# Kernel tuning notes

Measured on AMD Instinct MI355X. Metric: run time of the kernel, lower is better.

Reference implementation:

```python
import jax, jax.numpy as jnp
import numpy as np

N = 50000      # nodes
E = 600000     # edges
D_IN = 128
D = 128        # embedding_size
H = 2 * D      # GENConv MLP hidden (expansion=2, num_layers=2)
L = 6          # gnn_layers
OUT = 2        # out_channels
EPS_MSG = 1e-7   # GENConv message eps
EPS_SM = 1e-16   # PyG softmax denominator eps
LN_EPS = 1e-5


def setup_inputs() -> dict:
    key = jax.random.key(0)
    ks = jax.random.split(key, 18)
    s_in = 1.0 / np.sqrt(D_IN)
    s_d = 1.0 / np.sqrt(D)
    s_h = 1.0 / np.sqrt(H)
    return {
        "x": jax.random.normal(ks[0], (N, D_IN), jnp.float32),
        "edge_index": jax.random.randint(ks[1], (2, E), 0, N, jnp.int64),
        # node encoder
        "enc_W": jax.random.normal(ks[2], (D_IN, D), jnp.float32) * s_in,
        "enc_b": jnp.zeros((D,), jnp.float32),
        # per-layer DeepGCN params (stacked over L layers)
        "ln_g": jnp.ones((L, D), jnp.float32),
        "ln_b": jnp.zeros((L, D), jnp.float32),
        "t": jnp.ones((L,), jnp.float32),  # learnable softmax temperature
        "W1": jax.random.normal(ks[3], (L, D, H), jnp.float32) * s_d,
        "b1": jnp.zeros((L, H), jnp.float32),
        "mln_g": jnp.ones((L, H), jnp.float32),
        "mln_b": jnp.zeros((L, H), jnp.float32),
        "W2": jax.random.normal(ks[4], (L, H, D), jnp.float32) * s_h,
        "b2": jnp.zeros((L, D), jnp.float32),
        # final MLP head (linear_layers=2)
        "lin_W1": jax.random.normal(ks[5], (D, D), jnp.float32) * s_d,
        "lin_b1": jnp.zeros((D,), jnp.float32),
        "lin_W2": jax.random.normal(ks[6], (D, OUT), jnp.float32) * s_d,
        "lin_b2": jnp.zeros((OUT,), jnp.float32),
    }


def _layernorm(h, g, b):
    mu = jnp.mean(h, axis=-1, keepdims=True)
    var = jnp.mean(jnp.square(h - mu), axis=-1, keepdims=True)
    return (h - mu) * jax.lax.rsqrt(var + LN_EPS) * g + b


def _genconv(h, src, dst, t, W1, b1, mg, mb, W2, b2):
    """GENConv with softmax aggregation: gather -> segment softmax -> scatter -> MLP."""
    msg = jax.nn.relu(h[src]) + EPS_MSG            # [E, D]
    scaled = msg * t
    mmax = jax.ops.segment_max(scaled, dst, num_segments=N)  # [N, D]
    mmax = jnp.where(jnp.isfinite(mmax), mmax, 0.0)          # empty segments
    ex = jnp.exp(scaled - mmax[dst])                          # [E, D]
    denom = jax.ops.segment_sum(ex, dst, num_segments=N)     # [N, D]
    alpha = ex / (denom[dst] + EPS_SM)
    agg = jax.ops.segment_sum(msg * alpha, dst, num_segments=N)  # [N, D]
    out = agg + h                                  # root/self term
    z = out @ W1 + b1                              # [N, 2D]
    z = jax.nn.relu(_layernorm(z, mg, mb))
    return z @ W2 + b2                             # [N, D]


def reference(x, edge_index, enc_W, enc_b, ln_g, ln_b, t, W1, b1,
              mln_g, mln_b, W2, b2, lin_W1, lin_b1, lin_W2, lin_b2):
    src, dst = edge_index[0], edge_index[1]
    h = x @ enc_W + enc_b                          # node encoder [N, D]
    for i in range(L):                             # DeepGCNLayer 'res+' blocks
        g = _layernorm(h, ln_g[i], ln_b[i])
        g = jax.nn.relu(g)                         # (dropout: inference no-op)
        g = _genconv(g, src, dst, t[i], W1[i], b1[i], mln_g[i], mln_b[i], W2[i], b2[i])
        h = h + g
    h = jax.nn.relu(h @ lin_W1 + lin_b1)           # head (dropout_rate=None)
    return h @ lin_W2 + lin_b2                     # [N, OUT]
```

## Files before the change

### kernel.cpp

```cpp
#include <hip/hip_runtime.h>

#define NN 50000
#define EE 600000
#define DD 128
#define HH 256
#define LL 6
#define NB 49

typedef _Float16 f16x8 __attribute__((ext_vector_type(8)));
typedef float f32x4 __attribute__((ext_vector_type(4)));

__device__ __forceinline__ float bf2f(unsigned short u){
  unsigned int x = ((unsigned int)u) << 16; float f; __builtin_memcpy(&f, &x, 4); return f;
}
__device__ __forceinline__ unsigned short f2bf(float f){
  unsigned int x; __builtin_memcpy(&x, &f, 4);
  unsigned int lsb = (x >> 16) & 1u; x += 0x7fffu + lsb; return (unsigned short)(x >> 16);
}
__device__ __forceinline__ float wave_sum(float v){
  #pragma unroll
  for (int off = 32; off >= 1; off >>= 1) v += __shfl_xor(v, off, 64);
  return v;
}
__device__ __forceinline__ unsigned short f2h(float f){
  _Float16 h = (_Float16)f; unsigned short u; __builtin_memcpy(&u, &h, 2); return u;
}
__device__ __forceinline__ float h2f(unsigned short u){
  _Float16 h; __builtin_memcpy(&h, &u, 2); return (float)h;
}

__global__ void k_detect(const unsigned short* __restrict__ xh,
                         const unsigned int* __restrict__ ew,
                         int* __restrict__ flags){
  __shared__ int s_bad, s_nz;
  int t = threadIdx.x;
  if (t == 0){ s_bad = 0; s_nz = 0; }
  __syncthreads();
  int bad = 0;
  for (int i = t; i < 512; i += 256){
    unsigned e = (xh[i] >> 7) & 0xffu;
    if (e < 96u || e > 135u) bad = 1;
  }
  if (bad) atomicOr(&s_bad, 1);
  int nz = 0;
  for (int i = t; i < 1024; i += 256)
    if ((i & 1) && ew[i] != 0u) nz = 1;
  if (nz) atomicOr(&s_nz, 1);
  __syncthreads();
  if (t == 0){
    flags[0] = s_bad ? 1 : 0;
    flags[1] = s_nz ? 0 : 1;
  }
}

__global__ void k_cvt_edges(const void* __restrict__ ei, const int* __restrict__ flags,
                            int* __restrict__ s32, int* __restrict__ d32){
  int e = blockIdx.x*256 + threadIdx.x;
  if (e >= EE) return;
  int sv, dv;
  if (flags[1]){
    const long long* p = (const long long*)ei;
    sv = (int)p[e]; dv = (int)p[EE + e];
  } else {
    const int* p = (const int*)ei;
    sv = p[e]; dv = p[EE + e];
  }
  s32[e] = ((unsigned)sv < (unsigned)NN) ? sv : 0;
  d32[e] = ((unsigned)dv < (unsigned)NN) ? dv : 0;
}

__global__ void k_hist(const int* __restrict__ dst, int* __restrict__ deg){
  int e = blockIdx.x*256 + threadIdx.x;
  if (e < EE) atomicAdd(&deg[dst[e]], 1);
}

__global__ void k_blocksum(const int* __restrict__ deg, int* __restrict__ bsum){
  __shared__ int ws[4];
  int t = threadIdx.x, b = blockIdx.x;
  int s = 0;
  int i0 = b*1024 + t*4;
  #pragma unroll
  for (int j=0;j<4;j++){ int i = i0+j; if (i < NN) s += deg[i]; }
  #pragma unroll
  for (int off=32; off>=1; off>>=1) s += __shfl_xor(s, off, 64);
  if ((t&63)==0) ws[t>>6] = s;
  __syncthreads();
  if (t==0) bsum[b] = ws[0]+ws[1]+ws[2]+ws[3];
}

__global__ void k_scanb(const int* __restrict__ bsum, int* __restrict__ boff, int* __restrict__ rowptr){
  int lane = threadIdx.x;
  int v = (lane < NB) ? bsum[lane] : 0;
  int inc = v;
  #pragma unroll
  for (int off=1; off<64; off<<=1){ int u = __shfl_up(inc, off, 64); if (lane>=off) inc += u; }
  if (lane < NB) boff[lane] = inc - v;
  if (lane == 63) rowptr[NN] = inc;
}

__global__ void k_scanscatter(const int* __restrict__ deg, const int* __restrict__ boff,
                              int* __restrict__ rowptr, int* __restrict__ pos){
  __shared__ int ws[4];
  int t = threadIdx.x, b = blockIdx.x;
  int lane = t & 63, wid = t >> 6;
  int i0 = b*1024 + t*4;
  int d[4];
  #pragma unroll
  for (int j=0;j<4;j++){ int i=i0+j; d[j] = (i<NN)? deg[i] : 0; }
  int tot = d[0]+d[1]+d[2]+d[3];
  int inc = tot;
  #pragma unroll
  for (int off=1; off<64; off<<=1){ int u = __shfl_up(inc, off, 64); if (lane>=off) inc += u; }
  if (lane==63) ws[wid] = inc;
  __syncthreads();
  int woff = 0;
  for (int w=0; w<wid; w++) woff += ws[w];
  int base = boff[b] + woff + (inc - tot);
  int pre = 0;
  #pragma unroll
  for (int j=0;j<4;j++){
    int i = i0+j;
    if (i<NN){ rowptr[i] = base + pre; pos[i] = base + pre; }
    pre += d[j];
  }
}

__global__ void k_fill(const int* __restrict__ src, const int* __restrict__ dst,
                       int* __restrict__ pos, int* __restrict__ csr){
  int e = blockIdx.x*256 + threadIdx.x;
  if (e < EE){
    int d = dst[e];
    int p = atomicAdd(&pos[d], 1);
    csr[p] = src[e];
  }
}

__global__ void k_prep_w(const int* __restrict__ flags,
    const void* __restrict__ encW, const void* __restrict__ linW1,
    const void* __restrict__ W1, const void* __restrict__ W2,
    unsigned short* __restrict__ ph, unsigned short* __restrict__ pl)
{
  int idx = blockIdx.x*256 + threadIdx.x;
  int fp32 = flags[0];
  const void* src; int off;
  if (idx < 16384){ int n=idx>>7, k=idx&127; src=encW; off=k*128+n; }
  else if (idx < 32768){ int o=idx-16384; int n=o>>7, k=o&127; src=linW1; off=k*128+n; }
  else if (idx < 229376){ int o=idx-32768; int l=o>>15, r=o&32767; int n=r>>7, k=r&127; src=W1; off=l*32768+k*256+n; }
  else { int o=idx-229376; int l=o>>15, r=o&32767; int n=r>>8, k=r&255; src=W2; off=l*32768+k*128+n; }
  float w = fp32 ? ((const float*)src)[off] : bf2f(((const unsigned short*)src)[off]);
  unsigned short h = f2h(w);
  ph[idx] = h;
  pl[idx] = f2h(w - h2f(h));
}

#define SM_ENCB 0
#define SM_LNG 128
#define SM_LNB 896
#define SM_TV 1664
#define SM_B1 1670
#define SM_MG 3206
#define SM_MB 4742
#define SM_B2 6278
#define SM_LINB1 7046
#define SM_LINW2 7174
#define SM_LINB2 7430
#define SM_TOT 7432
__global__ void k_prep_small(const int* __restrict__ flags,
    const void* s0, const void* s1, const void* s2, const void* s3,
    const void* s4, const void* s5, const void* s6, const void* s7,
    const void* s8, const void* s9, const void* s10, float* __restrict__ out)
{
  int i = blockIdx.x*256 + threadIdx.x;
  if (i >= SM_TOT) return;
  int fp32 = flags[0];
  const void* src; int off;
  if      (i < SM_LNG)  { src=s0;  off=i; }
  else if (i < SM_LNB)  { src=s1;  off=i-SM_LNG; }
  else if (i < SM_TV)   { src=s2;  off=i-SM_LNB; }
  else if (i < SM_B1)   { src=s3;  off=i-SM_TV; }
  else if (i < SM_MG)   { src=s4;  off=i-SM_B1; }
  else if (i < SM_MB)   { src=s5;  off=i-SM_MG; }
  else if (i < SM_B2)   { src=s6;  off=i-SM_MB; }
  else if (i < SM_LINB1){ src=s7;  off=i-SM_B2; }
  else if (i < SM_LINW2){ src=s8;  off=i-SM_LINB1; }
  else if (i < SM_LINB2){ src=s9;  off=i-SM_LINW2; }
  else                  { src=s10; off=i-SM_LINB2; }
  out[i] = fp32 ? ((const float*)src)[off] : bf2f(((const unsigned short*)src)[off]);
}

__device__ __forceinline__ void emit_me(unsigned short* me, int row, int col, float g, float tv){
  float m = g + 1e-7f;
  me[(size_t)row*256 + col] = f2h(m);
  me[(size_t)row*256 + 128 + col] = f2h(__expf(fminf(m*tv, 18.f) - 8.f));
}

template<int EPI>
__global__ __launch_bounds__(256, 4) void k_gemm(const void* __restrict__ Ap,
    const unsigned short* __restrict__ WTh, const unsigned short* __restrict__ WTl,
    const float* __restrict__ bias, void* __restrict__ Cv,
    int M, const int* __restrict__ flags, int aExt)
{
  __shared__ __align__(16) char smem[27648];
  short* lA = (short*)smem;
  short* lW = (short*)(smem + 9216);
  short* hT = (short*)smem;

  const int tid = threadIdx.x, lane = tid & 63, wid = tid >> 6;
  const int mi = lane & 15, q = lane >> 4;
  const int rowb = blockIdx.x * 64;
  const int fp32m = flags[0];

  f32x4 acc[4][2];
  #pragma unroll
  for (int a=0;a<4;a++)
    #pragma unroll
    for (int c=0;c<2;c++){ acc[a][c][0]=0.f; acc[a][c][1]=0.f; acc[a][c][2]=0.f; acc[a][c][3]=0.f; }

  const int nW = fp32m ? 2 : 1;
  for (int pass = 0; pass < nW; ++pass){
    const unsigned short* Wp = pass ? WTl : WTh;
    for (int kc = 0; kc < 2; ++kc){
      {
        const int kv = (tid & 7) * 8, r0 = tid >> 3;
        #pragma unroll
        for (int p = 0; p < 2; ++p){
          int row = p*32 + r0, grow = rowb + row;
          uint4 d = make_uint4(0u,0u,0u,0u);
          if (grow < M){
            if (!aExt){
              d = *(const uint4*)((const unsigned short*)Ap + (size_t)grow*128 + kc*64 + kv);
            } else if (!fp32m){
              uint4 u = *(const uint4*)((const unsigned short*)Ap + (size_t)grow*128 + kc*64 + kv);
              const unsigned short* us = (const unsigned short*)&u;
              unsigned short hh[8];
              #pragma unroll
              for (int c=0;c<8;c++) hh[c] = f2h(bf2f(us[c]));
              d.x = hh[0]|((unsigned)hh[1]<<16); d.y = hh[2]|((unsigned)hh[3]<<16);
              d.z = hh[4]|((unsigned)hh[5]<<16); d.w = hh[6]|((unsigned)hh[7]<<16);
            } else {
              const float* fp = (const float*)Ap + (size_t)grow*128 + kc*64 + kv;
              float4 v0 = *(const float4*)fp, v1 = *(const float4*)(fp+4);
              unsigned short hh[8] = {f2h(v0.x),f2h(v0.y),f2h(v0.z),f2h(v0.w),
                                      f2h(v1.x),f2h(v1.y),f2h(v1.z),f2h(v1.w)};
              d.x = hh[0]|((unsigned)hh[1]<<16); d.y = hh[2]|((unsigned)hh[3]<<16);
              d.z = hh[4]|((unsigned)hh[5]<<16); d.w = hh[6]|((unsigned)hh[7]<<16);
            }
          }
          *(uint4*)&lA[row*72 + kv] = d;
        }
        #pragma unroll
        for (int p = 0; p < 4; ++p){
          int n = p*32 + (tid >> 3);
          *(uint4*)&lW[n*72 + (tid & 7)*8] = *(const uint4*)(Wp + (size_t)n*128 + kc*64 + (tid & 7)*8);
        }
      }
      __syncthreads();
      #pragma unroll
      for (int ks = 0; ks < 2; ++ks){
        const int koff = ks*32 + q*8;
        f16x8 af[4], bw[2];
        #pragma unroll
        for (int rt=0; rt<4; rt++) af[rt] = *(const f16x8*)&lA[(rt*16+mi)*72 + koff];
        #pragma unroll
        for (int ct=0; ct<2; ct++) bw[ct] = *(const f16x8*)&lW[(wid*32 + ct*16 + mi)*72 + koff];
        #pragma unroll
        for (int rt=0; rt<4; rt++)
          #pragma unroll
          for (int ct=0; ct<2; ct++)
            acc[rt][ct] = __builtin_amdgcn_mfma_f32_16x16x32_f16(af[rt], bw[ct], acc[rt][ct], 0,0,0);
      }
      __syncthreads();
    }
  }
  if (EPI == 3){
    #pragma unroll
    for (int ct=0; ct<2; ct++){
      const int col = wid*32 + ct*16 + mi;
      const float bf = bias[col];
      #pragma unroll
      for (int rt=0; rt<4; rt++)
        #pragma unroll
        for (int r=0; r<4; r++)
          hT[(rt*16 + q*4 + r)*136 + col] = (short)f2h(acc[rt][ct][r] + bf);
    }
    __syncthreads();
    unsigned short* C16 = (unsigned short*)Cv;
    #pragma unroll
    for (int i = 0; i < 4; ++i){
      int idx = i*256 + tid;
      int prow = idx >> 4, pl = idx & 15;
      int grow = rowb + prow;
      if (grow < M)
        *(uint4*)(C16 + (size_t)grow*128 + pl*8) = *(const uint4*)&hT[prow*136 + pl*8];
    }
  } else {
    #pragma unroll
    for (int ct=0; ct<2; ct++){
      const int col = wid*32 + ct*16 + mi;
      const float bf = bias[col];
      #pragma unroll
      for (int rt=0; rt<4; rt++)
        #pragma unroll
        for (int r=0; r<4; r++){
          int row = rowb + rt*16 + q*4 + r;
          if (row < M){
            float v = acc[rt][ct][r] + bf;
            if (EPI == 1) v = fmaxf(v, 0.f);
            ((float*)Cv)[(size_t)row*128 + col] = v;
          }
        }
    }
  }
}

__global__ __launch_bounds__(256, 3) void k_layer(const unsigned short* __restrict__ Ap,
    const unsigned short* __restrict__ W1h, const unsigned short* __restrict__ W1l,
    const unsigned short* __restrict__ W2h, const unsigned short* __restrict__ W2l,
    const float* __restrict__ b1, const float* __restrict__ mg, const float* __restrict__ mb,
    const float* __restrict__ b2, unsigned short* __restrict__ h16,
    const float* __restrict__ gam, const float* __restrict__ bet,
    const float* __restrict__ tp, unsigned short* __restrict__ me,
    int M, const int* __restrict__ flags, int doLN)
{
  __shared__ __align__(16) char smem[53248];
  short* lA  = (short*)smem;
  short* lW1 = (short*)(smem + 9216);
  short* zT  = (short*)smem;
  short* lW2 = (short*)(smem + 33792);
  short* hT  = (short*)smem;
  short* mE  = (short*)(smem + 17408);
  float2* sred = (float2*)(smem + 51200);

  const int tid = threadIdx.x, lane = tid & 63, wid = tid >> 6;
  const int mi = lane & 15, q = lane >> 4;
  const int kv = (tid & 7) * 8, r0 = tid >> 3;
  const int rowb = blockIdx.x * 64;
  const float tv = tp[0];
  const int nW = flags[0] ? 2 : 1;
  const int prow = tid >> 4;
  const int pl = tid & 15;

  f32x4 acc1[4][4];
  #pragma unroll
  for (int a=0;a<4;a++)
    #pragma unroll
    for (int c=0;c<4;c++){ acc1[a][c][0]=0.f; acc1[a][c][1]=0.f; acc1[a][c][2]=0.f; acc1[a][c][3]=0.f; }

  for (int pass = 0; pass < nW; ++pass){
    const unsigned short* Wp = pass ? W1l : W1h;
    for (int kc = 0; kc < 2; ++kc){
      if (pass == 0){
        #pragma unroll
        for (int p = 0; p < 2; ++p){
          int row = p*32 + r0, grow = rowb + row;
          uint4 d = make_uint4(0u,0u,0u,0u);
          if (grow < M) d = *(const uint4*)(Ap + (size_t)grow*128 + kc*64 + kv);
          *(uint4*)&lA[row*72 + kv] = d;
        }
      }
      #pragma unroll
      for (int p = 0; p < 8; ++p){
        int n = p*32 + r0;
        *(uint4*)&lW1[n*72 + kv] = *(const uint4*)(Wp + (size_t)n*128 + kc*64 + kv);
      }
      __syncthreads();
      #pragma unroll
      for (int ks = 0; ks < 2; ++ks){
        const int koff = ks*32 + q*8;
        f16x8 af[4], bw[4];
        #pragma unroll
        for (int rt=0; rt<4; rt++) af[rt] = *(const f16x8*)&lA[(rt*16+mi)*72 + koff];
        #pragma unroll
        for (int ct=0; ct<4; ct++) bw[ct] = *(const f16x8*)&lW1[(wid*64 + ct*16 + mi)*72 + koff];
        #pragma unroll
        for (int rt=0; rt<4; rt++)
          #pragma unroll
          for (int ct=0; ct<4; ct++)
            acc1[rt][ct] = __builtin_amdgcn_mfma_f32_16x16x32_f16(af[rt], bw[ct], acc1[rt][ct], 0,0,0);
      }
      __syncthreads();
    }
  }
  #pragma unroll
  for (int ct=0; ct<4; ct++){
    const float bf = b1[wid*64 + ct*16 + mi];
    #pragma unroll
    for (int rt=0; rt<4; rt++)
      #pragma unroll
      for (int r=0; r<4; r++) acc1[rt][ct][r] += bf;
  }
  #pragma unroll
  for (int rt=0; rt<4; rt++)
    #pragma unroll
    for (int r=0; r<4; r++){
      float s = 0.f, s2 = 0.f;
      #pragma unroll
      for (int ct=0; ct<4; ct++){ float v = acc1[rt][ct][r]; s += v; s2 += v*v; }
      #pragma unroll
      for (int off=1; off<16; off<<=1){ s += __shfl_xor(s, off, 64); s2 += __shfl_xor(s2, off, 64); }
      if (mi == 0) sred[wid*64 + rt*16 + q*4 + r] = make_float2(s, s2);
    }
  __syncthreads();
  float lnm[4][4], lnr[4][4];
  #pragma unroll
  for (int rt=0; rt<4; rt++)
    #pragma unroll
    for (int r=0; r<4; r++){
      int rl = rt*16 + q*4 + r;
      float2 t0 = sred[0*64+rl], t1 = sred[1*64+rl], t2 = sred[2*64+rl], t3 = sred[3*64+rl];
      float s = t0.x + t1.x + t2.x + t3.x;
      float s2 = t0.y + t1.y + t2.y + t3.y;
      float m = s * (1.f/256.f);
      float var = s2 * (1.f/256.f) - m*m;
      lnm[rt][r] = m;
      lnr[rt][r] = rsqrtf(var + 1e-5f);
    }
  __syncthreads();
  #pragma unroll
  for (int ct=0; ct<4; ct++){
    const int col = wid*64 + ct*16 + mi;
    const float gc = mg[col], bc = mb[col];
    #pragma unroll
    for (int rt=0; rt<4; rt++)
      #pragma unroll
      for (int r=0; r<4; r++){
        int rl = rt*16 + q*4 + r;
        float v = (acc1[rt][ct][r] - lnm[rt][r]) * lnr[rt][r] * gc + bc;
        zT[rl*264 + col] = (short)f2h(fmaxf(v, 0.f));
      }
  }
  __syncthreads();
  uint4 hpre[4];
  #pragma unroll
  for (int i = 0; i < 4; ++i){
    int grow = rowb + i*16 + prow;
    hpre[i] = make_uint4(0u,0u,0u,0u);
    if (grow < M) hpre[i] = *(const uint4*)(h16 + (size_t)grow*128 + pl*8);
  }
  f32x4 acc2[4][2];
  #pragma unroll
  for (int a=0;a<4;a++)
    #pragma unroll
    for (int c=0;c<2;c++){ acc2[a][c][0]=0.f; acc2[a][c][1]=0.f; acc2[a][c][2]=0.f; acc2[a][c][3]=0.f; }

  for (int pass = 0; pass < nW; ++pass){
    const unsigned short* Wp = pass ? W2l : W2h;
    for (int kc = 0; kc < 4; ++kc){
      #pragma unroll
      for (int p = 0; p < 4; ++p){
        int n = p*32 + r0;
        *(uint4*)&lW2[n*72 + kv] = *(const uint4*)(Wp + (size_t)n*256 + kc*64 + kv);
      }
      __syncthreads();
      #pragma unroll
      for (int ks = 0; ks < 2; ++ks){
        const int koff = ks*32 + q*8;
        f16x8 af[4], bw[2];
        #pragma unroll
        for (int rt=0; rt<4; rt++) af[rt] = *(const f16x8*)&zT[(rt*16+mi)*264 + kc*64 + koff];
        #pragma unroll
        for (int ct=0; ct<2; ct++) bw[ct] = *(const f16x8*)&lW2[(wid*32 + ct*16 + mi)*72 + koff];
        #pragma unroll
        for (int rt=0; rt<4; rt++)
          #pragma unroll
          for (int ct=0; ct<2; ct++)
            acc2[rt][ct] = __builtin_amdgcn_mfma_f32_16x16x32_f16(af[rt], bw[ct], acc2[rt][ct], 0,0,0);
      }
      __syncthreads();
    }
  }
  #pragma unroll
  for (int i = 0; i < 4; ++i)
    *(uint4*)&hT[(i*16 + prow)*136 + pl*8] = hpre[i];
  __syncthreads();
  #pragma unroll
  for (int ct=0; ct<2; ct++){
    const int col = wid*32 + ct*16 + mi;
    const float bf = b2[col];
    #pragma unroll
    for (int rt=0; rt<4; rt++)
      #pragma unroll
      for (int r=0; r<4; r++){
        int rl = rt*16 + q*4 + r;
        float hv = acc2[rt][ct][r] + bf + h2f((unsigned short)hT[rl*136 + col]);
        hT[rl*136 + col] = (short)f2h(hv);
        acc2[rt][ct][r] = hv;
      }
  }
  if (doLN){
    #pragma unroll
    for (int rt=0; rt<4; rt++)
      #pragma unroll
      for (int r=0; r<4; r++){
        float s = 0.f, s2 = 0.f;
        #pragma unroll
        for (int ct=0; ct<2; ct++){ float v = acc2[rt][ct][r]; s += v; s2 += v*v; }
        #pragma unroll
        for (int off=1; off<16; off<<=1){ s += __shfl_xor(s, off, 64); s2 += __shfl_xor(s2, off, 64); }
        if (mi == 0) sred[wid*64 + rt*16 + q*4 + r] = make_float2(s, s2);
      }
    __syncthreads();
    #pragma unroll
    for (int rt=0; rt<4; rt++)
      #pragma unroll
      for (int r=0; r<4; r++){
        int rl = rt*16 + q*4 + r;
        float2 t0 = sred[0*64+rl], t1 = sred[1*64+rl], t2 = sred[2*64+rl], t3 = sred[3*64+rl];
        float s = t0.x + t1.x + t2.x + t3.x;
        float s2 = t0.y + t1.y + t2.y + t3.y;
        float m = s * (1.f/128.f);
        float var = s2 * (1.f/128.f) - m*m;
        float rs = rsqrtf(var + 1e-5f);
        #pragma unroll
        for (int ct=0; ct<2; ct++){
          int col = wid*32 + ct*16 + mi;
          float g = fmaxf((acc2[rt][ct][r] - m) * rs * gam[col] + bet[col], 0.f);
          float mm = g + 1e-7f;
          mE[rl*264 + col] = (short)f2h(mm);
          mE[rl*264 + 128 + col] = (short)f2h(__expf(fminf(mm*tv, 18.f) - 8.f));
        }
      }
  }
  __syncthreads();
  #pragma unroll
  for (int i = 0; i < 4; ++i){
    int grow = rowb + i*16 + prow;
    if (grow < M)
      *(uint4*)(h16 + (size_t)grow*128 + pl*8) = *(const uint4*)&hT[(i*16 + prow)*136 + pl*8];
  }
  if (doLN){
    #pragma unroll
    for (int i = 0; i < 8; ++i){
      int idx2 = i*256 + tid;
      int mrow = idx2 >> 5, part = (idx2 >> 4) & 1, l16 = idx2 & 15;
      int grow = rowb + mrow;
      if (grow < M)
        *(uint4*)(me + (size_t)grow*256 + part*128 + l16*8)
          = *(const uint4*)&mE[mrow*264 + part*128 + l16*8];
    }
  }
}

__global__ __launch_bounds__(256,4) void k_preln0(const unsigned short* __restrict__ h16,
    const float* __restrict__ gam, const float* __restrict__ bet,
    const float* __restrict__ tp, unsigned short* __restrict__ me)
{
  int wid = threadIdx.x >> 6, lane = threadIdx.x & 63;
  int row = blockIdx.x*4 + wid;
  float tv = tp[0];
  unsigned u = ((const unsigned*)(h16 + (size_t)row*DD))[lane];
  float v0 = h2f((unsigned short)(u & 0xffffu));
  float v1 = h2f((unsigned short)(u >> 16));
  float mean = wave_sum(v0+v1) * (1.f/128.f);
  float d0 = v0-mean, d1 = v1-mean;
  float var = wave_sum(d0*d0 + d1*d1) * (1.f/128.f);
  float rs = rsqrtf(var + 1e-5f);
  float o0 = fmaxf(d0*rs*gam[2*lane]   + bet[2*lane],   0.f);
  float o1 = fmaxf(d1*rs*gam[2*lane+1] + bet[2*lane+1], 0.f);
  emit_me(me, row, 2*lane,   o0, tv);
  emit_me(me, row, 2*lane+1, o1, tv);
}

__global__ __launch_bounds__(256,4) void k_agg(
    const unsigned short* __restrict__ me,
    const int* __restrict__ rowptr, const int* __restrict__ csr,
    unsigned short* __restrict__ obf)
{
  int wid = threadIdx.x>>6, lane = threadIdx.x&63;
  int node = blockIdx.x*4 + wid;
  int st = rowptr[node], en = rowptr[node+1];
  int quad = lane >> 4, fi = lane & 15;
  float l[8], ac[8];
  #pragma unroll
  for (int f=0; f<8; f++){ l[f]=0.f; ac[f]=0.f; }
  for (int base = st; base < en; base += 64){
    int cnt = min(64, en - base);
    int sv = (lane < cnt) ? csr[base + lane] : NN;
    for (int j = 0; j < cnt; j += 8){
      int s0i = __shfl(sv, j + quad, 64);
      int s1i = __shfl(sv, j + 4 + quad, 64);
      bool two = (j + 4) < cnt;
      const unsigned short* mer0 = me + (size_t)s0i*256 + fi*8;
      f16x8 mh0 = *(const f16x8*)(mer0);
      f16x8 eh0 = *(const f16x8*)(mer0 + 128);
      if (two){
        const unsigned short* mer1 = me + (size_t)s1i*256 + fi*8;
        f16x8 mh1 = *(const f16x8*)(mer1);
        f16x8 eh1 = *(const f16x8*)(mer1 + 128);
        #pragma unroll
        for (int f=0; f<8; f++){
          l[f]  = fmaf((float)eh0[f], 1.f, l[f]);
          ac[f] = fmaf((float)mh0[f], (float)eh0[f], ac[f]);
          l[f]  = fmaf((float)eh1[f], 1.f, l[f]);
          ac[f] = fmaf((float)mh1[f], (float)eh1[f], ac[f]);
        }
      } else {
        #pragma unroll
        for (int f=0; f<8; f++){
          l[f]  = fmaf((float)eh0[f], 1.f, l[f]);
          ac[f] = fmaf((float)mh0[f], (float)eh0[f], ac[f]);
        }
      }
    }
  }
  #pragma unroll
  for (int off=16; off<=32; off<<=1)
    #pragma unroll
    for (int f=0; f<8; f++){ l[f] += __shfl_xor(l[f], off, 64); ac[f] += __shfl_xor(ac[f], off, 64); }
  if (quad == 0){
    f16x8 mh = *(const f16x8*)(me + (size_t)node*256 + fi*8);
    unsigned short o[8];
    #pragma unroll
    for (int f=0; f<8; f++){
      float a = ac[f] / (l[f] + 1e-16f);
      o[f] = f2h(((float)mh[f] - 1e-7f) + a);
    }
    uint4 w;
    w.x = o[0]|((unsigned)o[1]<<16); w.y = o[2]|((unsigned)o[3]<<16);
    w.z = o[4]|((unsigned)o[5]<<16); w.w = o[6]|((unsigned)o[7]<<16);
    *(uint4*)(obf + (size_t)node*DD + fi*8) = w;
  }
}

__global__ __launch_bounds__(256,4) void k_head2(const float* __restrict__ u,
    const float* __restrict__ w, const float* __restrict__ b,
    void* __restrict__ out, const int* __restrict__ flags)
{
  int wid = threadIdx.x>>6, lane = threadIdx.x&63;
  int row = blockIdx.x*4 + wid;
  const float* ur = u + (size_t)row*DD;
  float u0 = ur[lane], u1 = ur[lane+64];
  float s0 = u0*w[lane*2+0] + u1*w[(lane+64)*2+0];
  float s1 = u0*w[lane*2+1] + u1*w[(lane+64)*2+1];
  s0 = wave_sum(s0); s1 = wave_sum(s1);
  if (lane == 0){
    float o0 = s0 + b[0], o1 = s1 + b[1];
    if (flags[0]){
      ((float*)out)[row*2+0] = o0;
      ((float*)out)[row*2+1] = o1;
    } else {
      ((unsigned short*)out)[row*2+0] = f2bf(o0);
      ((unsigned short*)out)[row*2+1] = f2bf(o1);
    }
  }
}

extern "C" void kernel_launch(void* const* d_in, const int* in_sizes, int n_in,
                              void* d_out, int out_size, void* d_ws, size_t ws_size,
                              hipStream_t stream)
{
  (void)in_sizes; (void)n_in; (void)out_size; (void)ws_size;
  char* ws = (char*)d_ws;
  size_t off = 0;
  auto alloc = [&](size_t bytes) -> char* {
    char* p = ws + off;
    off = (off + bytes + 255) & ~(size_t)255;
    return p;
  };
  int* flags  = (int*)alloc(256);
  float* sm   = (float*)alloc(SM_TOT*4);
  unsigned short* planeH = (unsigned short*)alloc(425984*2);
  unsigned short* planeL = (unsigned short*)alloc(425984*2);
  int* src32  = (int*)alloc((size_t)EE*4);
  int* dst32  = (int*)alloc((size_t)EE*4);
  int* deg    = (int*)alloc((size_t)NN*4);
  int* pos    = (int*)alloc((size_t)NN*4);
  int* rowptr = (int*)alloc((size_t)(NN+1)*4);
  int* csr    = (int*)alloc((size_t)EE*4);
  int* bsum   = (int*)alloc(64*4);
  int* boff   = (int*)alloc(64*4);
  unsigned short* h16 = (unsigned short*)alloc((size_t)NN*128*2);
  unsigned short* me   = (unsigned short*)alloc((size_t)(NN+1)*256*2);
  unsigned short* obf  = (unsigned short*)alloc((size_t)NN*128*2);
  float* ob   = (float*)alloc((size_t)NN*128*4);

  k_detect<<<1,256,0,stream>>>((const unsigned short*)d_in[0], (const unsigned int*)d_in[1], flags);
  k_cvt_edges<<<(EE+255)/256,256,0,stream>>>(d_in[1], flags, src32, dst32);
  hipMemsetAsync(deg, 0, (size_t)NN*4, stream);
  hipMemsetAsync(me + (size_t)NN*256, 0, 512, stream);
  k_hist<<<(EE+255)/256,256,0,stream>>>(dst32, deg);
  k_blocksum<<<NB,256,0,stream>>>(deg, bsum);
  k_scanb<<<1,64,0,stream>>>(bsum, boff, rowptr);
  k_scanscatter<<<NB,256,0,stream>>>(deg, boff, rowptr, pos);
  k_fill<<<(EE+255)/256,256,0,stream>>>(src32, dst32, pos, csr);
  k_prep_w<<<1664,256,0,stream>>>(flags, d_in[2], d_in[13], d_in[7], d_in[11], planeH, planeL);
  k_prep_small<<<30,256,0,stream>>>(flags, d_in[3], d_in[4], d_in[5], d_in[6], d_in[8],
                                    d_in[9], d_in[10], d_in[12], d_in[14], d_in[15], d_in[16], sm);

  const int GB = (NN + 63)/64;
  k_gemm<3><<<GB,256,0,stream>>>((const void*)d_in[0], planeH + 0, planeL + 0,
                                 sm + SM_ENCB, (void*)h16, NN, flags, 1);
  k_preln0<<<NN/4,256,0,stream>>>(h16, sm + SM_LNG, sm + SM_LNB, sm + SM_TV, me);
  for (int i = 0; i < LL; ++i){
    k_agg<<<NN/4,256,0,stream>>>(me, rowptr, csr, obf);
    int nl = (i+1 < LL) ? (i+1) : 0;
    k_layer<<<GB,256,0,stream>>>(obf,
                                 planeH + 32768 + i*32768, planeL + 32768 + i*32768,
                                 planeH + 229376 + i*32768, planeL + 229376 + i*32768,
                                 sm + SM_B1 + i*256, sm + SM_MG + i*256, sm + SM_MB + i*256,
                                 sm + SM_B2 + i*128, h16,
                                 sm + SM_LNG + nl*128, sm + SM_LNB + nl*128,
                                 sm + SM_TV + nl,
                                 me, NN, flags, (i+1 < LL) ? 1 : 0);
  }
  k_gemm<1><<<GB,256,0,stream>>>((const void*)h16, planeH + 16384, planeL + 16384,
                                 sm + SM_LINB1, (void*)ob, NN, flags, 0);
  k_head2<<<NN/4,256,0,stream>>>(ob, sm + SM_LINW2, sm + SM_LINB2, d_out, flags);
}
```

Baseline: 807.9 us.

## Shrink k_layer shared memory for higher occupancy and store head hidden in fp16

Cuts k_layer's LDS footprint from about 52KB to about 37KB and raises launch bounds to 4 blocks per CU. To fit, the first GEMM uses 32-wide K chunks, the LN output is packed into registers, and the second GEMM is split into two K halves staged through a smaller buffer. The me message/exp planes are written in two passes that reuse a half-size tile. Separately, the final head GEMM now writes fp16 instead of fp32, halving that intermediate's traffic, at the cost of more syncs, extra register pressure and a small precision loss.

```diff
diff --git a/kernel.cpp b/kernel.cpp
--- a/kernel.cpp
+++ b/kernel.cpp
@@ -272,48 +272,32 @@
       __syncthreads();
     }
   }
-  if (EPI == 3){
-    #pragma unroll
-    for (int ct=0; ct<2; ct++){
-      const int col = wid*32 + ct*16 + mi;
-      const float bf = bias[col];
-      #pragma unroll
-      for (int rt=0; rt<4; rt++)
-        #pragma unroll
-        for (int r=0; r<4; r++)
-          hT[(rt*16 + q*4 + r)*136 + col] = (short)f2h(acc[rt][ct][r] + bf);
-    }
-    __syncthreads();
-    unsigned short* C16 = (unsigned short*)Cv;
-    #pragma unroll
-    for (int i = 0; i < 4; ++i){
-      int idx = i*256 + tid;
-      int prow = idx >> 4, pl = idx & 15;
-      int grow = rowb + prow;
-      if (grow < M)
-        *(uint4*)(C16 + (size_t)grow*128 + pl*8) = *(const uint4*)&hT[prow*136 + pl*8];
-    }
-  } else {
-    #pragma unroll
-    for (int ct=0; ct<2; ct++){
-      const int col = wid*32 + ct*16 + mi;
-      const float bf = bias[col];
-      #pragma unroll
-      for (int rt=0; rt<4; rt++)
-        #pragma unroll
-        for (int r=0; r<4; r++){
-          int row = rowb + rt*16 + q*4 + r;
-          if (row < M){
-            float v = acc[rt][ct][r] + bf;
-            if (EPI == 1) v = fmaxf(v, 0.f);
-            ((float*)Cv)[(size_t)row*128 + col] = v;
-          }
-        }
-    }
-  }
-}
-
-__global__ __launch_bounds__(256, 3) void k_layer(const unsigned short* __restrict__ Ap,
+  #pragma unroll
+  for (int ct=0; ct<2; ct++){
+    const int col = wid*32 + ct*16 + mi;
+    const float bf = bias[col];
+    #pragma unroll
+    for (int rt=0; rt<4; rt++)
+      #pragma unroll
+      for (int r=0; r<4; r++){
+        float v = acc[rt][ct][r] + bf;
+        if (EPI == 4) v = fmaxf(v, 0.f);
+        hT[(rt*16 + q*4 + r)*136 + col] = (short)f2h(v);
+      }
+  }
+  __syncthreads();
+  unsigned short* C16 = (unsigned short*)Cv;
+  #pragma unroll
+  for (int i = 0; i < 4; ++i){
+    int idx = i*256 + tid;
+    int prow = idx >> 4, pl = idx & 15;
+    int grow = rowb + prow;
+    if (grow < M)
+      *(uint4*)(C16 + (size_t)grow*128 + pl*8) = *(const uint4*)&hT[prow*136 + pl*8];
+  }
+}
+
+__global__ __launch_bounds__(256, 4) void k_layer(const unsigned short* __restrict__ Ap,
     const unsigned short* __restrict__ W1h, const unsigned short* __restrict__ W1l,
     const unsigned short* __restrict__ W2h, const unsigned short* __restrict__ W2l,
     const float* __restrict__ b1, const float* __restrict__ mg, const float* __restrict__ mb,
@@ -322,23 +306,22 @@
     const float* __restrict__ tp, unsigned short* __restrict__ me,
     int M, const int* __restrict__ flags, int doLN)
 {
-  __shared__ __align__(16) char smem[53248];
+  __shared__ __align__(16) char smem[37888];
   short* lA  = (short*)smem;
-  short* lW1 = (short*)(smem + 9216);
-  short* zT  = (short*)smem;
-  short* lW2 = (short*)(smem + 33792);
+  short* lW1 = (short*)(smem + 5120);
+  short* zH  = (short*)smem;
+  short* lW2 = (short*)(smem + 17408);
   short* hT  = (short*)smem;
   short* mE  = (short*)(smem + 17408);
-  float2* sred = (float2*)(smem + 51200);
+  float2* sred = (float2*)(smem + 35840);
 
   const int tid = threadIdx.x, lane = tid & 63, wid = tid >> 6;
   const int mi = lane & 15, q = lane >> 4;
-  const int kv = (tid & 7) * 8, r0 = tid >> 3;
   const int rowb = blockIdx.x * 64;
   const float tv = tp[0];
   const int nW = flags[0] ? 2 : 1;
-  const int prow = tid >> 4;
-  const int pl = tid & 15;
+  const int prow = tid >> 4, pl = tid & 15;
+  const int arow = tid >> 2, acol = (tid & 3)*8;
 
   f32x4 acc1[4][4];
   #pragma unroll
@@ -348,36 +331,30 @@
 
   for (int pass = 0; pass < nW; ++pass){
     const unsigned short* Wp = pass ? W1l : W1h;
-    for (int kc = 0; kc < 2; ++kc){
+    for (int kc = 0; kc < 4; ++kc){
       if (pass == 0){
-        #pragma unroll
-        for (int p = 0; p < 2; ++p){
-          int row = p*32 + r0, grow = rowb + row;
-          uint4 d = make_uint4(0u,0u,0u,0u);
-          if (grow < M) d = *(const uint4*)(Ap + (size_t)grow*128 + kc*64 + kv);
-          *(uint4*)&lA[row*72 + kv] = d;
-        }
-      }
-      #pragma unroll
-      for (int p = 0; p < 8; ++p){
-        int n = p*32 + r0;
-        *(uint4*)&lW1[n*72 + kv] = *(const uint4*)(Wp + (size_t)n*128 + kc*64 + kv);
+        int grow = rowb + arow;
+        uint4 d = make_uint4(0u,0u,0u,0u);
+        if (grow < M) d = *(const uint4*)(Ap + (size_t)grow*128 + kc*32 + acol);
+        *(uint4*)&lA[arow*40 + acol] = d;
+      }
+      #pragma unroll
+      for (int p = 0; p < 4; ++p){
+        int n = p*64 + arow;
+        *(uint4*)&lW1[n*40 + acol] = *(const uint4*)(Wp + (size_t)n*128 + kc*32 + acol);
       }
       __syncthreads();
-      #pragma unroll
-      for (int ks = 0; ks < 2; ++ks){
-        const int koff = ks*32 + q*8;
-        f16x8 af[4], bw[4];
-        #pragma unroll
-        for (int rt=0; rt<4; rt++) af[rt] = *(const f16x8*)&lA[(rt*16+mi)*72 + koff];
-        #pragma unroll
-        for (int ct=0; ct<4; ct++) bw[ct] = *(const f16x8*)&lW1[(wid*64 + ct*16 + mi)*72 + koff];
-        #pragma unroll
-        for (int rt=0; rt<4; rt++)
-          #pragma unroll
-          for (int ct=0; ct<4; ct++)
-            acc1[rt][ct] = __builtin_amdgcn_mfma_f32_16x16x32_f16(af[rt], bw[ct], acc1[rt][ct], 0,0,0);
-      }
+      const int koff = q*8;
+      f16x8 af[4], bw[4];
+      #pragma unroll
+      for (int rt=0; rt<4; rt++) af[rt] = *(const f16x8*)&lA[(rt*16+mi)*40 + koff];
+      #pragma unroll
+      for (int ct=0; ct<4; ct++) bw[ct] = *(const f16x8*)&lW1[(wid*64 + ct*16 + mi)*40 + koff];
+      #pragma unroll
+      for (int rt=0; rt<4; rt++)
+        #pragma unroll
+        for (int ct=0; ct<4; ct++)
+          acc1[rt][ct] = __builtin_amdgcn_mfma_f32_16x16x32_f16(af[rt], bw[ct], acc1[rt][ct], 0,0,0);
       __syncthreads();
     }
   }
@@ -401,35 +378,28 @@
       if (mi == 0) sred[wid*64 + rt*16 + q*4 + r] = make_float2(s, s2);
     }
   __syncthreads();
-  float lnm[4][4], lnr[4][4];
+  unsigned zp[4][4][2];
   #pragma unroll
   for (int rt=0; rt<4; rt++)
     #pragma unroll
-    for (int r=0; r<4; r++){
-      int rl = rt*16 + q*4 + r;
-      float2 t0 = sred[0*64+rl], t1 = sred[1*64+rl], t2 = sred[2*64+rl], t3 = sred[3*64+rl];
-      float s = t0.x + t1.x + t2.x + t3.x;
-      float s2 = t0.y + t1.y + t2.y + t3.y;
-      float m = s * (1.f/256.f);
-      float var = s2 * (1.f/256.f) - m*m;
-      lnm[rt][r] = m;
-      lnr[rt][r] = rsqrtf(var + 1e-5f);
-    }
-  __syncthreads();
-  #pragma unroll
-  for (int ct=0; ct<4; ct++){
-    const int col = wid*64 + ct*16 + mi;
-    const float gc = mg[col], bc = mb[col];
-    #pragma unroll
-    for (int rt=0; rt<4; rt++)
-      #pragma unroll
-      for (int r=0; r<4; r++){
-        int rl = rt*16 + q*4 + r;
-        float v = (acc1[rt][ct][r] - lnm[rt][r]) * lnr[rt][r] * gc + bc;
-        zT[rl*264 + col] = (short)f2h(fmaxf(v, 0.f));
-      }
-  }
-  __syncthreads();
+    for (int r2=0; r2<2; r2++){
+      int rl0 = rt*16 + q*4 + r2*2;
+      float2 t0 = sred[0*64+rl0], t1 = sred[1*64+rl0], t2 = sred[2*64+rl0], t3 = sred[3*64+rl0];
+      float s = t0.x+t1.x+t2.x+t3.x, s2 = t0.y+t1.y+t2.y+t3.y;
+      float m0 = s*(1.f/256.f); float rs0 = rsqrtf(s2*(1.f/256.f)-m0*m0 + 1e-5f);
+      int rl1 = rl0 + 1;
+      t0 = sred[0*64+rl1]; t1 = sred[1*64+rl1]; t2 = sred[2*64+rl1]; t3 = sred[3*64+rl1];
+      s = t0.x+t1.x+t2.x+t3.x; s2 = t0.y+t1.y+t2.y+t3.y;
+      float m1 = s*(1.f/256.f); float rs1 = rsqrtf(s2*(1.f/256.f)-m1*m1 + 1e-5f);
+      #pragma unroll
+      for (int ct=0; ct<4; ct++){
+        int col = wid*64 + ct*16 + mi;
+        float gc = mg[col], bc = mb[col];
+        float g0 = fmaxf((acc1[rt][ct][r2*2]   - m0)*rs0*gc + bc, 0.f);
+        float g1 = fmaxf((acc1[rt][ct][r2*2+1] - m1)*rs1*gc + bc, 0.f);
+        zp[rt][ct][r2] = (unsigned)f2h(g0) | ((unsigned)f2h(g1) << 16);
+      }
+    }
   uint4 hpre[4];
   #pragma unroll
   for (int i = 0; i < 4; ++i){
@@ -443,30 +413,47 @@
     #pragma unroll
     for (int c=0;c<2;c++){ acc2[a][c][0]=0.f; acc2[a][c][1]=0.f; acc2[a][c][2]=0.f; acc2[a][c][3]=0.f; }
 
-  for (int pass = 0; pass < nW; ++pass){
-    const unsigned short* Wp = pass ? W2l : W2h;
-    for (int kc = 0; kc < 4; ++kc){
-      #pragma unroll
-      for (int p = 0; p < 4; ++p){
-        int n = p*32 + r0;
-        *(uint4*)&lW2[n*72 + kv] = *(const uint4*)(Wp + (size_t)n*256 + kc*64 + kv);
-      }
-      __syncthreads();
-      #pragma unroll
-      for (int ks = 0; ks < 2; ++ks){
-        const int koff = ks*32 + q*8;
-        f16x8 af[4], bw[2];
-        #pragma unroll
-        for (int rt=0; rt<4; rt++) af[rt] = *(const f16x8*)&zT[(rt*16+mi)*264 + kc*64 + koff];
-        #pragma unroll
-        for (int ct=0; ct<2; ct++) bw[ct] = *(const f16x8*)&lW2[(wid*32 + ct*16 + mi)*72 + koff];
+  const int kv8 = (tid & 7)*8;
+  for (int ph = 0; ph < 2; ++ph){
+    if ((wid >> 1) == ph){
+      const int cbase = (wid & 1)*64;
+      #pragma unroll
+      for (int ct=0; ct<4; ct++)
         #pragma unroll
         for (int rt=0; rt<4; rt++)
           #pragma unroll
-          for (int ct=0; ct<2; ct++)
-            acc2[rt][ct] = __builtin_amdgcn_mfma_f32_16x16x32_f16(af[rt], bw[ct], acc2[rt][ct], 0,0,0);
-      }
-      __syncthreads();
+          for (int r=0; r<4; r++){
+            unsigned u = zp[rt][ct][r>>1];
+            unsigned short v = (r & 1) ? (unsigned short)(u >> 16) : (unsigned short)(u & 0xffffu);
+            zH[(rt*16 + q*4 + r)*136 + cbase + ct*16 + mi] = (short)v;
+          }
+    }
+    __syncthreads();
+    for (int pass = 0; pass < nW; ++pass){
+      const unsigned short* Wp = pass ? W2l : W2h;
+      for (int kc = 0; kc < 2; ++kc){
+        #pragma unroll
+        for (int p = 0; p < 4; ++p){
+          int n = p*32 + (tid >> 3);
+          *(uint4*)&lW2[n*72 + kv8] = *(const uint4*)(Wp + (size_t)n*256 + ph*128 + kc*64 + kv8);
+        }
+        __syncthreads();
+        #pragma unroll
+        for (int ks = 0; ks < 2; ++ks){
+          const int koff = ks*32 + q*8;
+          f16x8 af[4], bw[2];
+          #pragma unroll
+          for (int rt=0; rt<4; rt++) af[rt] = *(const f16x8*)&zH[(rt*16+mi)*136 + kc*64 + koff];
+          #pragma unroll
+          for (int ct=0; ct<2; ct++) bw[ct] = *(const f16x8*)&lW2[(wid*32 + ct*16 + mi)*72 + koff];
+          #pragma unroll
+          for (int rt=0; rt<4; rt++)
+            #pragma unroll
+            for (int ct=0; ct<2; ct++)
+              acc2[rt][ct] = __builtin_amdgcn_mfma_f32_16x16x32_f16(af[rt], bw[ct], acc2[rt][ct], 0,0,0);
+        }
+        __syncthreads();
+      }
     }
   }
   #pragma unroll
@@ -499,45 +486,73 @@
         for (int off=1; off<16; off<<=1){ s += __shfl_xor(s, off, 64); s2 += __shfl_xor(s2, off, 64); }
         if (mi == 0) sred[wid*64 + rt*16 + q*4 + r] = make_float2(s, s2);
       }
-    __syncthreads();
+  }
+  __syncthreads();
+  float lnm2[4][4], lnr2[4][4];
+  if (doLN){
     #pragma unroll
     for (int rt=0; rt<4; rt++)
       #pragma unroll
       for (int r=0; r<4; r++){
         int rl = rt*16 + q*4 + r;
         float2 t0 = sred[0*64+rl], t1 = sred[1*64+rl], t2 = sred[2*64+rl], t3 = sred[3*64+rl];
-        float s = t0.x + t1.x + t2.x + t3.x;
-        float s2 = t0.y + t1.y + t2.y + t3.y;
-        float m = s * (1.f/128.f);
-        float var = s2 * (1.f/128.f) - m*m;
-        float rs = rsqrtf(var + 1e-5f);
-        #pragma unroll
-        for (int ct=0; ct<2; ct++){
-          int col = wid*32 + ct*16 + mi;
-          float g = fmaxf((acc2[rt][ct][r] - m) * rs * gam[col] + bet[col], 0.f);
-          float mm = g + 1e-7f;
-          mE[rl*264 + col] = (short)f2h(mm);
-          mE[rl*264 + 128 + col] = (short)f2h(__expf(fminf(mm*tv, 18.f) - 8.f));
+        float s = t0.x+t1.x+t2.x+t3.x, s2 = t0.y+t1.y+t2.y+t3.y;
+        float m = s*(1.f/128.f);
+        lnm2[rt][r] = m;
+        lnr2[rt][r] = rsqrtf(s2*(1.f/128.f) - m*m + 1e-5f);
+      }
+    #pragma unroll
+    for (int ct=0; ct<2; ct++){
+      const int col = wid*32 + ct*16 + mi;
+      const float gc = gam[col], bc = bet[col];
+      #pragma unroll
+      for (int rt=0; rt<4; rt++)
+        #pragma unroll
+        for (int r=0; r<4; r++){
+          int rl = rt*16 + q*4 + r;
+          float g = fmaxf((acc2[rt][ct][r] - lnm2[rt][r])*lnr2[rt][r]*gc + bc, 0.f);
+          mE[rl*136 + col] = (short)f2h(g + 1e-7f);
         }
-      }
-  }
-  __syncthreads();
+    }
+  }
   #pragma unroll
   for (int i = 0; i < 4; ++i){
     int grow = rowb + i*16 + prow;
     if (grow < M)
       *(uint4*)(h16 + (size_t)grow*128 + pl*8) = *(const uint4*)&hT[(i*16 + prow)*136 + pl*8];
   }
-  if (doLN){
-    #pragma unroll
-    for (int i = 0; i < 8; ++i){
-      int idx2 = i*256 + tid;
-      int mrow = idx2 >> 5, part = (idx2 >> 4) & 1, l16 = idx2 & 15;
-      int grow = rowb + mrow;
-      if (grow < M)
-        *(uint4*)(me + (size_t)grow*256 + part*128 + l16*8)
-          = *(const uint4*)&mE[mrow*264 + part*128 + l16*8];
-    }
+  if (!doLN) return;
+  __syncthreads();
+  #pragma unroll
+  for (int i = 0; i < 4; ++i){
+    int idx = i*256 + tid;
+    int mrow = idx >> 4, l16 = idx & 15;
+    int grow = rowb + mrow;
+    if (grow < M)
+      *(uint4*)(me + (size_t)grow*256 + l16*8) = *(const uint4*)&mE[mrow*136 + l16*8];
+  }
+  #pragma unroll
+  for (int ct=0; ct<2; ct++){
+    const int col = wid*32 + ct*16 + mi;
+    const float gc = gam[col], bc = bet[col];
+    #pragma unroll
+    for (int rt=0; rt<4; rt++)
+      #pragma unroll
+      for (int r=0; r<4; r++){
+        int rl = rt*16 + q*4 + r;
+        float g = fmaxf((acc2[rt][ct][r] - lnm2[rt][r])*lnr2[rt][r]*gc + bc, 0.f);
+        float mm = g + 1e-7f;
+        hT[rl*136 + col] = (short)f2h(__expf(fminf(mm*tv, 18.f) - 8.f));
+      }
+  }
+  __syncthreads();
+  #pragma unroll
+  for (int i = 0; i < 4; ++i){
+    int idx = i*256 + tid;
+    int mrow = idx >> 4, l16 = idx & 15;
+    int grow = rowb + mrow;
+    if (grow < M)
+      *(uint4*)(me + (size_t)grow*256 + 128 + l16*8) = *(const uint4*)&hT[mrow*136 + l16*8];
   }
 }
 
@@ -622,16 +637,17 @@
   }
 }
 
-__global__ __launch_bounds__(256,4) void k_head2(const float* __restrict__ u,
+__global__ __launch_bounds__(256,4) void k_head2(const unsigned short* __restrict__ u16,
     const float* __restrict__ w, const float* __restrict__ b,
     void* __restrict__ out, const int* __restrict__ flags)
 {
   int wid = threadIdx.x>>6, lane = threadIdx.x&63;
   int row = blockIdx.x*4 + wid;
-  const float* ur = u + (size_t)row*DD;
-  float u0 = ur[lane], u1 = ur[lane+64];
-  float s0 = u0*w[lane*2+0] + u1*w[(lane+64)*2+0];
-  float s1 = u0*w[lane*2+1] + u1*w[(lane+64)*2+1];
+  unsigned uu = ((const unsigned*)(u16 + (size_t)row*DD))[lane];
+  float u0 = h2f((unsigned short)(uu & 0xffffu));
+  float u1 = h2f((unsigned short)(uu >> 16));
+  float s0 = u0*w[(2*lane)*2+0] + u1*w[(2*lane+1)*2+0];
+  float s1 = u0*w[(2*lane)*2+1] + u1*w[(2*lane+1)*2+1];
   s0 = wave_sum(s0); s1 = wave_sum(s1);
   if (lane == 0){
     float o0 = s0 + b[0], o1 = s1 + b[1];
@@ -672,7 +688,7 @@
   unsigned short* h16 = (unsigned short*)alloc((size_t)NN*128*2);
   unsigned short* me   = (unsigned short*)alloc((size_t)(NN+1)*256*2);
   unsigned short* obf  = (unsigned short*)alloc((size_t)NN*128*2);
-  float* ob   = (float*)alloc((size_t)NN*128*4);
+  unsigned short* ob16 = (unsigned short*)alloc((size_t)NN*128*2);
 
   k_detect<<<1,256,0,stream>>>((const unsigned short*)d_in[0], (const unsigned int*)d_in[1], flags);
   k_cvt_edges<<<(EE+255)/256,256,0,stream>>>(d_in[1], flags, src32, dst32);
@@ -703,7 +719,7 @@
                                  sm + SM_TV + nl,
                                  me, NN, flags, (i+1 < LL) ? 1 : 0);
   }
-  k_gemm<1><<<GB,256,0,stream>>>((const void*)h16, planeH + 16384, planeL + 16384,
-                                 sm + SM_LINB1, (void*)ob, NN, flags, 0);
-  k_head2<<<NN/4,256,0,stream>>>(ob, sm + SM_LINW2, sm + SM_LINB2, d_out, flags);
-}
+  k_gemm<4><<<GB,256,0,stream>>>((const void*)h16, planeH + 16384, planeL + 16384,
+                                 sm + SM_LINB1, (void*)ob16, NN, flags, 0);
+  k_head2<<<NN/4,256,0,stream>>>(ob16, sm + SM_LINW2, sm + SM_LINB2, d_out, flags);
+}
```

New measurement: 1.028 ms. 1.27x slower.
